# Optimization experiments

Hardware: AMD Instinct MI355X
Metric: run time of the kernel (lower is better)

Reference implementation:

```python
import jax, jax.numpy as jnp
import numpy as np

DIM = 192
HEAD_DIM = 32
HEADS = DIM // HEAD_DIM  # 6
H = W = 56
WS = 7            # window size
SS = 3            # shift size
L = WS * WS       # tokens per window = 49
NH, NW = H // WS, W // WS
NWIN = NH * NW    # windows per image = 64
SCALE = HEAD_DIM ** -0.5


def _rel_indices():
    # matches ShiftedWindowAttention.get_indices
    a = np.arange(WS)
    y1, x1, y2, x2 = np.meshgrid(a, a, a, a, indexing='ij')
    idx = (y1 - y2 + WS - 1) * (2 * WS - 1) + (x1 - x2 + WS - 1)
    return idx.reshape(-1)  # [WS^4] = [L*L]


def _shift_mask():
    # matches ShiftedWindowAttention.generate_mask -> bool [NWIN, L, L]
    region = np.zeros((H, W), dtype=np.int32)
    slices = [slice(0, -WS), slice(-WS, -SS), slice(-SS, None)]
    r = 0
    for i in slices:
        for j in slices:
            region[i, j] = r
            r += 1
    win = region.reshape(NH, WS, NW, WS).transpose(0, 2, 1, 3).reshape(NWIN, L)
    return (win[:, None, :] - win[:, :, None]) != 0


_REL_IDX = _rel_indices()
_MASK = _shift_mask()


def setup_inputs() -> dict:
    key = jax.random.key(0)
    ks = jax.random.split(key, 4)
    B = 32
    return {
        'x': jax.random.normal(ks[0], (B, H * W, DIM), jnp.float32),
        'w_qkv': jax.random.normal(ks[1], (3 * DIM, DIM), jnp.float32) * 0.02,
        'b_qkv': jnp.zeros((3 * DIM,), jnp.float32),
        'w_out': jax.random.normal(ks[2], (DIM, DIM), jnp.float32) * 0.02,
        'b_out': jnp.zeros((DIM,), jnp.float32),
        'pos_enc': jax.random.normal(ks[3], (HEADS, (2 * WS - 1) ** 2), jnp.float32) * 0.02,
    }


def reference(x, w_qkv, b_qkv, w_out, b_out, pos_enc):
    B = x.shape[0]
    # to windows (with cyclic shift)
    xg = x.reshape(B, H, W, DIM)
    xg = jnp.roll(xg, (-SS, -SS), axis=(1, 2))
    xw = xg.reshape(B, NH, WS, NW, WS, DIM).transpose(0, 1, 3, 2, 4, 5)
    xw = xw.reshape(B * NWIN, L, DIM)
    # qkv projection: torch Linear -> x @ W^T + b
    qkv = xw @ w_qkv.T + b_qkv                      # [BW, L, 3*DIM]
    qkv = qkv.reshape(B * NWIN, L, 3, HEADS, HEAD_DIM)
    qkv = qkv.transpose(2, 0, 3, 1, 4)              # [3, BW, heads, L, hd]
    q, k, v = qkv[0], qkv[1], qkv[2]
    # attention scores + gathered relative position bias
    att = jnp.einsum('whid,whjd->whij', q, k) * SCALE  # [BW, heads, L, L]
    rel = pos_enc[:, _REL_IDX].reshape(HEADS, L, L)    # gather per head
    att = att + rel
    # shift mask
    mask = jnp.asarray(_MASK)                          # [NWIN, L, L]
    att = att.reshape(B, NWIN, HEADS, L, L)
    att = jnp.where(mask[None, :, None, :, :], -jnp.inf, att)
    att = att.reshape(B * NWIN, HEADS, L, L)
    att = jax.nn.softmax(att, axis=-1)
    # weighted values, merge heads
    out = jnp.einsum('whij,whjd->whid', att, v)        # [BW, heads, L, hd]
    out = out.transpose(0, 2, 1, 3).reshape(B * NWIN, L, DIM)
    out = out @ w_out.T + b_out
    # from windows (undo shift)
    out = out.reshape(B, NH, NW, WS, WS, DIM).transpose(0, 1, 3, 2, 4, 5)
    out = out.reshape(B, H, W, DIM)
    out = jnp.roll(out, (SS, SS), axis=(1, 2))
    return out.reshape(B, H * W, DIM)
```

## Files before the change

### kernel.cpp

```cpp
#include <hip/hip_runtime.h>
#include <hip/hip_bf16.h>
#include <cstddef>
#include <cstdint>

typedef _Float16 half_t;
typedef _Float16 half8  __attribute__((ext_vector_type(8)));
typedef _Float16 half4v __attribute__((ext_vector_type(4)));
typedef float    f32x4  __attribute__((ext_vector_type(4)));

#define SCALE 0.17677669529663687f


__global__ __launch_bounds__(256) void convert_w(
    const float* __restrict__ w_qkv, const float* __restrict__ w_out,
    half_t* __restrict__ wq, half_t* __restrict__ wo)
{
    int i = blockIdx.x * 256 + threadIdx.x;
    if (i < 110592) {
        int u8 = i >> 3, e = i & 7;
        int c  = u8 & 15;
        int g  = (u8 >> 4) & 3;
        int ks = (u8 >> 6) % 6;
        int ct = u8 / 384;
        wq[i] = (half_t)w_qkv[(16 * ct + c) * 192 + ks * 32 + g * 8 + e];
    } else {
        int j = i - 110592;
        if (j < 36864) {
            int u8 = j >> 3, e = j & 7;
            int c  = u8 & 15;
            int g  = (u8 >> 4) & 3;
            int ks = (u8 >> 6) % 6;
            int q  = u8 / 384;
            wo[j] = (half_t)w_out[(16 * q + c) * 192 + ks * 32 + g * 8 + e];
        }
    }
}

__global__ __launch_bounds__(256) void build_bias(
    const float* __restrict__ pos_enc, half_t* __restrict__ mb)
{
    int idx = blockIdx.x * 256 + threadIdx.x;
    int j   = idx & 63;
    int i   = (idx >> 6) & 63;
    int hmc = idx >> 12;
    int h   = hmc % 6, mc = hmc / 6;
    float v = -60000.f;
    if (i < 49 && j < 49) {
        int yi = i / 7, xi = i - 7 * yi;
        int yj = j / 7, xj = j - 7 * yj;
        int ri = ((mc & 2) ? (yi < 4 ? 1 : 2) : 0) * 3 + ((mc & 1) ? (xi < 4 ? 1 : 2) : 0);
        int rj = ((mc & 2) ? (yj < 4 ? 1 : 2) : 0) * 3 + ((mc & 1) ? (xj < 4 ? 1 : 2) : 0);
        if (ri == rj) v = pos_enc[h * 169 + (yi - yj + 6) * 13 + (xi - xj + 6)];
    }
    mb[idx] = (half_t)v;
}

__global__ __launch_bounds__(512, 4) void swin_fused(
    const float*  __restrict__ x,
    const half_t* __restrict__ wqfrag,
    const float*  __restrict__ b_qkv,
    const half_t* __restrict__ mb16,
    const half_t* __restrict__ wofrag,
    const float*  __restrict__ b_out,
    float* __restrict__ out)
{
    __shared__ half_t sQ[2][2][64][34];
    __shared__ half_t sK[2][2][64][34];
    __shared__ half_t sV2[2][2][4][2][16][16];
    __shared__ half_t sA2[12][64][16];

    const int w    = blockIdx.x;
    const int b    = w >> 6, win = w & 63, nh = win >> 3, nw = win & 7;
    const int tid  = threadIdx.x;
    const int wave = tid >> 6, lane = tid & 63;
    const int c    = lane & 15, g = lane >> 4;
    const int cf = wave >> 1, mh = wave & 1;
    const int ti = wave & 3, hf = wave >> 2;
    const int i_tok = 16 * ti + c;
    const int mc = 2 * (nh == 7) + (nw == 7);

    half8 xf[2][6];
    #pragma unroll
    for (int t = 0; t < 2; ++t) {
        int tok = 32 * mh + 16 * t + c;
        if (tok < 49) {
            int ty = tok / 7, tx = tok - ty * 7;
            int sy = nh * 7 + ty + 3; if (sy >= 56) sy -= 56;
            int sx = nw * 7 + tx + 3; if (sx >= 56) sx -= 56;
            const float* xr = x + ((size_t)b * 3136 + sy * 56 + sx) * 192 + g * 8;
            #pragma unroll
            for (int ks = 0; ks < 6; ++ks) {
                float4 v0 = *(const float4*)(xr + ks * 32);
                float4 v1 = *(const float4*)(xr + ks * 32 + 4);
                xf[t][ks] = (half8){(half_t)v0.x, (half_t)v0.y, (half_t)v0.z, (half_t)v0.w,
                                    (half_t)v1.x, (half_t)v1.y, (half_t)v1.z, (half_t)v1.w};
            }
        } else {
            #pragma unroll
            for (int ks = 0; ks < 6; ++ks)
                xf[t][ks] = (half8){(half_t)0.f, (half_t)0.f, (half_t)0.f, (half_t)0.f,
                                    (half_t)0.f, (half_t)0.f, (half_t)0.f, (half_t)0.f};
        }
    }

    #pragma unroll
    for (int pp = 0; pp < 3; ++pp) {
        const int buf = pp & 1;

        {
            f32x4 acc[3][2];
            #pragma unroll
            for (int q = 0; q < 3; ++q) {
                acc[q][0] = (f32x4){0.f, 0.f, 0.f, 0.f};
                acc[q][1] = (f32x4){0.f, 0.f, 0.f, 0.f};
            }
            #pragma unroll
            for (int ks = 0; ks < 6; ++ks) {
                #pragma unroll
                for (int q = 0; q < 3; ++q) {
                    const int cc   = 3 * cf + q;
                    const int kind = cc >> 2, sub = cc & 3;
                    const int hh   = sub >> 1, dh = sub & 1;
                    const int ct   = kind * 12 + (2 * pp + hh) * 2 + dh;
                    half8 bF = *(const half8*)(wqfrag + (((size_t)ct * 6 + ks) * 64 + g * 16 + c) * 8);
                    acc[q][0] = __builtin_amdgcn_mfma_f32_16x16x32_f16(xf[0][ks], bF, acc[q][0], 0, 0, 0);
                    acc[q][1] = __builtin_amdgcn_mfma_f32_16x16x32_f16(xf[1][ks], bF, acc[q][1], 0, 0, 0);
                }
            }
            #pragma unroll
            for (int q = 0; q < 3; ++q) {
                const int cc   = 3 * cf + q;
                const int kind = cc >> 2, sub = cc & 3;
                const int hh   = sub >> 1, dh = sub & 1;
                const int ct   = kind * 12 + (2 * pp + hh) * 2 + dh;
                const float bias = b_qkv[16 * ct + c];
                if (kind == 2) {
                    #pragma unroll
                    for (int t = 0; t < 2; ++t) {
                        half4v pv = (half4v){(half_t)(acc[q][t][0] + bias), (half_t)(acc[q][t][1] + bias),
                                             (half_t)(acc[q][t][2] + bias), (half_t)(acc[q][t][3] + bias)};
                        *(half4v*)&sV2[buf][hh][2 * mh + t][dh][c][4 * g] = pv;
                    }
                } else {
                    #pragma unroll
                    for (int t = 0; t < 2; ++t) {
                        #pragma unroll
                        for (int r = 0; r < 4; ++r) {
                            int tok = 32 * mh + 16 * t + 4 * g + r;
                            half_t vv = (half_t)(acc[q][t][r] + bias);
                            if (kind == 0) sQ[buf][hh][tok][dh * 16 + c] = vv;
                            else           sK[buf][hh][tok][dh * 16 + c] = vv;
                        }
                    }
                }
            }
        }
        __syncthreads();

        {
            const int h = 2 * pp + hf;
            const half_t* mrow = mb16 + ((size_t)(mc * 6 + h) * 64 + i_tok) * 64;
            half4v bfr[4];
            #pragma unroll
            for (int tj = 0; tj < 4; ++tj)
                bfr[tj] = *(const half4v*)(mrow + 16 * tj + 4 * g);

            half8 qf = *(const half8*)&sQ[buf][hf][i_tok][g * 8];
            f32x4 st[4];
            #pragma unroll
            for (int tj = 0; tj < 4; ++tj) {
                half8 kf = *(const half8*)&sK[buf][hf][16 * tj + c][g * 8];
                f32x4 z = (f32x4){0.f, 0.f, 0.f, 0.f};
                st[tj] = __builtin_amdgcn_mfma_f32_16x16x32_f16(kf, qf, z, 0, 0, 0);
            }
            #pragma unroll
            for (int tj = 0; tj < 4; ++tj)
                #pragma unroll
                for (int r = 0; r < 4; ++r)
                    st[tj][r] = st[tj][r] * SCALE + (float)bfr[tj][r];

            float m = st[0][0];
            #pragma unroll
            for (int tj = 0; tj < 4; ++tj)
                #pragma unroll
                for (int r = 0; r < 4; ++r) m = fmaxf(m, st[tj][r]);
            m = fmaxf(m, __shfl_xor(m, 16));
            m = fmaxf(m, __shfl_xor(m, 32));
            float sum = 0.f;
            #pragma unroll
            for (int tj = 0; tj < 4; ++tj)
                #pragma unroll
                for (int r = 0; r < 4; ++r) {
                    float e = __expf(st[tj][r] - m);
                    st[tj][r] = e;
                    sum += e;
                }
            sum += __shfl_xor(sum, 16);
            sum += __shfl_xor(sum, 32);
            float inv = 1.0f / sum;
            half4v pa[4];
            #pragma unroll
            for (int tj = 0; tj < 4; ++tj)
                pa[tj] = (half4v){(half_t)(st[tj][0] * inv), (half_t)(st[tj][1] * inv),
                                  (half_t)(st[tj][2] * inv), (half_t)(st[tj][3] * inv)};

            f32x4 o0 = (f32x4){0.f, 0.f, 0.f, 0.f};
            f32x4 o1 = (f32x4){0.f, 0.f, 0.f, 0.f};
            #pragma unroll
            for (int tj = 0; tj < 4; ++tj) {
                half4v v0 = *(const half4v*)&sV2[buf][hf][tj][0][c][4 * g];
                half4v v1 = *(const half4v*)&sV2[buf][hf][tj][1][c][4 * g];
                o0 = __builtin_amdgcn_mfma_f32_16x16x16f16(v0, pa[tj], o0, 0, 0, 0);
                o1 = __builtin_amdgcn_mfma_f32_16x16x16f16(v1, pa[tj], o1, 0, 0, 0);
            }
            *(half4v*)&sA2[2 * h][i_tok][4 * g] =
                (half4v){(half_t)o0[0], (half_t)o0[1], (half_t)o0[2], (half_t)o0[3]};
            *(half4v*)&sA2[2 * h + 1][i_tok][4 * g] =
                (half4v){(half_t)o1[0], (half_t)o1[1], (half_t)o1[2], (half_t)o1[3]};
        }
    }
    __syncthreads();

    {
        f32x4 pacc[6];
        float bo[6];
        #pragma unroll
        for (int q = 0; q < 6; ++q) {
            pacc[q] = (f32x4){0.f, 0.f, 0.f, 0.f};
            bo[q] = b_out[16 * (6 * hf + q) + c];
        }
        #pragma unroll
        for (int ks = 0; ks < 6; ++ks) {
            half8 aF = *(const half8*)&sA2[2 * ks + (g >> 1)][i_tok][(g & 1) * 8];
            #pragma unroll
            for (int q = 0; q < 6; ++q) {
                int ct = 6 * hf + q;
                half8 bF = *(const half8*)(wofrag + ((size_t)(ct * 6 + ks) * 64 + lane) * 8);
                pacc[q] = __builtin_amdgcn_mfma_f32_16x16x32_f16(aF, bF, pacc[q], 0, 0, 0);
            }
        }
        #pragma unroll
        for (int r = 0; r < 4; ++r) {
            int tok = 16 * ti + g * 4 + r;
            if (tok < 49) {
                int ty = tok / 7, tx = tok - ty * 7;
                int dy = nh * 7 + ty + 3; if (dy >= 56) dy -= 56;
                int dx = nw * 7 + tx + 3; if (dx >= 56) dx -= 56;
                float* op = out + ((size_t)b * 3136 + dy * 56 + dx) * 192;
                #pragma unroll
                for (int q = 0; q < 6; ++q)
                    op[16 * (6 * hf + q) + c] = pacc[q][r] + bo[q];
            }
        }
    }
}

extern "C" void kernel_launch(void* const* d_in, const int* in_sizes, int n_in,
                              void* d_out, int out_size, void* d_ws, size_t ws_size,
                              hipStream_t stream) {
    const float* x       = (const float*)d_in[0];
    const float* w_qkv   = (const float*)d_in[1];
    const float* b_qkv   = (const float*)d_in[2];
    const float* w_out   = (const float*)d_in[3];
    const float* b_out   = (const float*)d_in[4];
    const float* pos_enc = (const float*)d_in[5];
    float* out = (float*)d_out;

    half_t* wqf  = (half_t*)d_ws;
    half_t* wof  = (half_t*)((char*)d_ws + 221184);
    half_t* mb16 = (half_t*)((char*)d_ws + 294912);

    convert_w<<<dim3(576), dim3(256), 0, stream>>>(w_qkv, w_out, wqf, wof);
    build_bias<<<dim3(384), dim3(256), 0, stream>>>(pos_enc, mb16);
    swin_fused<<<dim3(2048), dim3(512), 0, stream>>>(
        x, wqf, b_qkv, mb16, wof, b_out, out);
}
```

Before: 148.6 us.

## Keep Q in registers, store K/V in MFMA fragment layout, one barrier

Each wave now projects Q, K and V for its own 16-token tile and three heads at once, keeping Q fragments in registers and writing K/V into shared memory already in MFMA operand order. The padded last tile (tokens 48..63) is stored as a single broadcast row. This replaces the three per-head-pair phases, each ending in a __syncthreads, with a single barrier. It also prefetches the mask/bias rows one head ahead and writes the attention output directly in the fragment layout the output projection reads. The cost is more register pressure from 6 Q fragments, and redundant weight loads since each wave reads its own heads' weights.

```diff
diff --git a/kernel.cpp b/kernel.cpp
--- a/kernel.cpp
+++ b/kernel.cpp
@@ -64,158 +64,212 @@
     const float*  __restrict__ b_out,
     float* __restrict__ out)
 {
-    __shared__ half_t sQ[2][2][64][34];
-    __shared__ half_t sK[2][2][64][34];
-    __shared__ half_t sV2[2][2][4][2][16][16];
-    __shared__ half_t sA2[12][64][16];
+    __shared__ __align__(16) half_t sKf[6 * 2 * 3 * 256];
+    __shared__ __align__(16) half_t sVf[6 * 2 * 3 * 256];
+    __shared__ __align__(16) half_t sKt[6 * 2 * 16];
+    __shared__ __align__(16) half_t sVt[6 * 2 * 16];
+    __shared__ __align__(16) half_t sAf[6 * 4 * 64 * 8];
 
     const int w    = blockIdx.x;
     const int b    = w >> 6, win = w & 63, nh = win >> 3, nw = win & 7;
     const int tid  = threadIdx.x;
     const int wave = tid >> 6, lane = tid & 63;
     const int c    = lane & 15, g = lane >> 4;
-    const int cf = wave >> 1, mh = wave & 1;
-    const int ti = wave & 3, hf = wave >> 2;
+    const int ti   = wave & 3, hf = wave >> 2;
     const int i_tok = 16 * ti + c;
-    const int mc = 2 * (nh == 7) + (nw == 7);
-
-    half8 xf[2][6];
+    const int mc   = 2 * (nh == 7) + (nw == 7);
+
+    half8 xf[6];
+    if (i_tok < 49) {
+        int ty = i_tok / 7, tx = i_tok - ty * 7;
+        int sy = nh * 7 + ty + 3; if (sy >= 56) sy -= 56;
+        int sx = nw * 7 + tx + 3; if (sx >= 56) sx -= 56;
+        const float* xr = x + ((size_t)b * 3136 + sy * 56 + sx) * 192 + g * 8;
+        #pragma unroll
+        for (int ks = 0; ks < 6; ++ks) {
+            float4 v0 = *(const float4*)(xr + ks * 32);
+            float4 v1 = *(const float4*)(xr + ks * 32 + 4);
+            xf[ks] = (half8){(half_t)v0.x, (half_t)v0.y, (half_t)v0.z, (half_t)v0.w,
+                             (half_t)v1.x, (half_t)v1.y, (half_t)v1.z, (half_t)v1.w};
+        }
+    } else {
+        #pragma unroll
+        for (int ks = 0; ks < 6; ++ks)
+            xf[ks] = (half8){(half_t)0.f, (half_t)0.f, (half_t)0.f, (half_t)0.f,
+                             (half_t)0.f, (half_t)0.f, (half_t)0.f, (half_t)0.f};
+    }
+
+    half4v qf[3][2];
     #pragma unroll
-    for (int t = 0; t < 2; ++t) {
-        int tok = 32 * mh + 16 * t + c;
-        if (tok < 49) {
-            int ty = tok / 7, tx = tok - ty * 7;
-            int sy = nh * 7 + ty + 3; if (sy >= 56) sy -= 56;
-            int sx = nw * 7 + tx + 3; if (sx >= 56) sx -= 56;
-            const float* xr = x + ((size_t)b * 3136 + sy * 56 + sx) * 192 + g * 8;
-            #pragma unroll
-            for (int ks = 0; ks < 6; ++ks) {
-                float4 v0 = *(const float4*)(xr + ks * 32);
-                float4 v1 = *(const float4*)(xr + ks * 32 + 4);
-                xf[t][ks] = (half8){(half_t)v0.x, (half_t)v0.y, (half_t)v0.z, (half_t)v0.w,
-                                    (half_t)v1.x, (half_t)v1.y, (half_t)v1.z, (half_t)v1.w};
-            }
-        } else {
+    for (int p = 0; p < 3; ++p) {
+        #pragma unroll
+        for (int dh = 0; dh < 2; ++dh) {
+            const int h  = 3 * hf + p;
+            const int ct = h * 2 + dh;
+            const half_t* wp = wqfrag + ((size_t)ct * 384 + lane) * 8;
+            half8 bfm[6];
+            #pragma unroll
+            for (int ks = 0; ks < 6; ++ks) bfm[ks] = *(const half8*)(wp + ks * 512);
+            f32x4 a0 = (f32x4){0.f, 0.f, 0.f, 0.f};
             #pragma unroll
             for (int ks = 0; ks < 6; ++ks)
-                xf[t][ks] = (half8){(half_t)0.f, (half_t)0.f, (half_t)0.f, (half_t)0.f,
-                                    (half_t)0.f, (half_t)0.f, (half_t)0.f, (half_t)0.f};
+                a0 = __builtin_amdgcn_mfma_f32_16x16x32_f16(bfm[ks], xf[ks], a0, 0, 0, 0);
+            float4 bq = *(const float4*)(b_qkv + 16 * ct + 4 * g);
+            half4v pv = (half4v){(half_t)(a0[0] + bq.x), (half_t)(a0[1] + bq.y),
+                                 (half_t)(a0[2] + bq.z), (half_t)(a0[3] + bq.w)};
+            if (ti < 3) {
+                qf[p][dh] = pv;
+            } else {
+                union { half4v h; int i2[2]; } u; u.h = pv;
+                u.i2[0] = __shfl(u.i2[0], lane & 48);
+                u.i2[1] = __shfl(u.i2[1], lane & 48);
+                qf[p][dh] = u.h;
+            }
         }
     }
 
     #pragma unroll
-    for (int pp = 0; pp < 3; ++pp) {
-        const int buf = pp & 1;
-
+    for (int p = 0; p < 3; ++p) {
+        #pragma unroll
+        for (int dh = 0; dh < 2; ++dh) {
+            const int h  = 3 * hf + p;
+            const int ct = 12 + h * 2 + dh;
+            const half_t* wp = wqfrag + ((size_t)ct * 384 + lane) * 8;
+            half8 bfm[6];
+            #pragma unroll
+            for (int ks = 0; ks < 6; ++ks) bfm[ks] = *(const half8*)(wp + ks * 512);
+            f32x4 a0 = (f32x4){0.f, 0.f, 0.f, 0.f};
+            #pragma unroll
+            for (int ks = 0; ks < 6; ++ks)
+                a0 = __builtin_amdgcn_mfma_f32_16x16x32_f16(bfm[ks], xf[ks], a0, 0, 0, 0);
+            float4 bq = *(const float4*)(b_qkv + 16 * ct + 4 * g);
+            half4v pv = (half4v){(half_t)(a0[0] + bq.x), (half_t)(a0[1] + bq.y),
+                                 (half_t)(a0[2] + bq.z), (half_t)(a0[3] + bq.w)};
+            if (ti < 3) {
+                *(half4v*)&sKf[h * 1536 + dh * 768 + ti * 256 + lane * 4] = pv;
+            } else if (c == 0) {
+                *(half4v*)&sKt[(h * 2 + dh) * 16 + 4 * g] = pv;
+            }
+        }
+    }
+
+    #pragma unroll
+    for (int p = 0; p < 3; ++p) {
+        #pragma unroll
+        for (int dh = 0; dh < 2; ++dh) {
+            const int h  = 3 * hf + p;
+            const int ct = 24 + h * 2 + dh;
+            const half_t* wp = wqfrag + ((size_t)ct * 384 + lane) * 8;
+            half8 bfm[6];
+            #pragma unroll
+            for (int ks = 0; ks < 6; ++ks) bfm[ks] = *(const half8*)(wp + ks * 512);
+            f32x4 a0 = (f32x4){0.f, 0.f, 0.f, 0.f};
+            #pragma unroll
+            for (int ks = 0; ks < 6; ++ks)
+                a0 = __builtin_amdgcn_mfma_f32_16x16x32_f16(xf[ks], bfm[ks], a0, 0, 0, 0);
+            const float bv = b_qkv[16 * ct + c];
+            if (ti < 3) {
+                half4v pv = (half4v){(half_t)(a0[0] + bv), (half_t)(a0[1] + bv),
+                                     (half_t)(a0[2] + bv), (half_t)(a0[3] + bv)};
+                *(half4v*)&sVf[h * 1536 + dh * 768 + ti * 256 + lane * 4] = pv;
+            } else if (g == 0) {
+                sVt[(h * 2 + dh) * 16 + c] = (half_t)(a0[0] + bv);
+            }
+        }
+    }
+    __syncthreads();
+
+    half4v bA[4], bB[4];
+    {
+        const half_t* mrow = mb16 + ((size_t)(mc * 6 + 3 * hf) * 64 + i_tok) * 64;
+        #pragma unroll
+        for (int tj = 0; tj < 4; ++tj)
+            bA[tj] = *(const half4v*)(mrow + 16 * tj + 4 * g);
+    }
+
+    #pragma unroll
+    for (int p = 0; p < 3; ++p) {
+        const int h = 3 * hf + p;
+        if (p == 0) {
+            const half_t* mrow = mb16 + ((size_t)(mc * 6 + h + 1) * 64 + i_tok) * 64;
+            #pragma unroll
+            for (int tj = 0; tj < 4; ++tj) bB[tj] = *(const half4v*)(mrow + 16 * tj + 4 * g);
+        }
+        if (p == 1) {
+            const half_t* mrow = mb16 + ((size_t)(mc * 6 + h + 1) * 64 + i_tok) * 64;
+            #pragma unroll
+            for (int tj = 0; tj < 4; ++tj) bA[tj] = *(const half4v*)(mrow + 16 * tj + 4 * g);
+        }
+        const half4v* bf = (p == 1) ? bB : bA;
+
+        f32x4 st[4];
+        #pragma unroll
+        for (int tj = 0; tj < 4; ++tj) {
+            half4v ka0, ka1;
+            if (tj < 3) {
+                ka0 = *(const half4v*)&sKf[h * 1536 + 0 * 768 + tj * 256 + lane * 4];
+                ka1 = *(const half4v*)&sKf[h * 1536 + 1 * 768 + tj * 256 + lane * 4];
+            } else {
+                ka0 = *(const half4v*)&sKt[(h * 2 + 0) * 16 + 4 * g];
+                ka1 = *(const half4v*)&sKt[(h * 2 + 1) * 16 + 4 * g];
+            }
+            f32x4 z = (f32x4){0.f, 0.f, 0.f, 0.f};
+            z = __builtin_amdgcn_mfma_f32_16x16x16f16(ka0, qf[p][0], z, 0, 0, 0);
+            st[tj] = __builtin_amdgcn_mfma_f32_16x16x16f16(ka1, qf[p][1], z, 0, 0, 0);
+        }
+        #pragma unroll
+        for (int tj = 0; tj < 4; ++tj)
+            #pragma unroll
+            for (int r = 0; r < 4; ++r)
+                st[tj][r] = st[tj][r] * SCALE + (float)bf[tj][r];
+
+        float m = st[0][0];
+        #pragma unroll
+        for (int tj = 0; tj < 4; ++tj)
+            #pragma unroll
+            for (int r = 0; r < 4; ++r) m = fmaxf(m, st[tj][r]);
+        m = fmaxf(m, __shfl_xor(m, 16));
+        m = fmaxf(m, __shfl_xor(m, 32));
+        float sum = 0.f;
+        #pragma unroll
+        for (int tj = 0; tj < 4; ++tj)
+            #pragma unroll
+            for (int r = 0; r < 4; ++r) {
+                float e = __expf(st[tj][r] - m);
+                st[tj][r] = e;
+                sum += e;
+            }
+        sum += __shfl_xor(sum, 16);
+        sum += __shfl_xor(sum, 32);
+        float inv = 1.0f / sum;
+        half4v pa[4];
+        #pragma unroll
+        for (int tj = 0; tj < 4; ++tj)
+            pa[tj] = (half4v){(half_t)(st[tj][0] * inv), (half_t)(st[tj][1] * inv),
+                              (half_t)(st[tj][2] * inv), (half_t)(st[tj][3] * inv)};
+
+        f32x4 o0 = (f32x4){0.f, 0.f, 0.f, 0.f};
+        f32x4 o1 = (f32x4){0.f, 0.f, 0.f, 0.f};
+        #pragma unroll
+        for (int tj = 0; tj < 3; ++tj) {
+            half4v v0 = *(const half4v*)&sVf[h * 1536 + 0 * 768 + tj * 256 + lane * 4];
+            half4v v1 = *(const half4v*)&sVf[h * 1536 + 1 * 768 + tj * 256 + lane * 4];
+            o0 = __builtin_amdgcn_mfma_f32_16x16x16f16(v0, pa[tj], o0, 0, 0, 0);
+            o1 = __builtin_amdgcn_mfma_f32_16x16x16f16(v1, pa[tj], o1, 0, 0, 0);
+        }
         {
-            f32x4 acc[3][2];
-            #pragma unroll
-            for (int q = 0; q < 3; ++q) {
-                acc[q][0] = (f32x4){0.f, 0.f, 0.f, 0.f};
-                acc[q][1] = (f32x4){0.f, 0.f, 0.f, 0.f};
-            }
-            #pragma unroll
-            for (int ks = 0; ks < 6; ++ks) {
-                #pragma unroll
-                for (int q = 0; q < 3; ++q) {
-                    const int cc   = 3 * cf + q;
-                    const int kind = cc >> 2, sub = cc & 3;
-                    const int hh   = sub >> 1, dh = sub & 1;
-                    const int ct   = kind * 12 + (2 * pp + hh) * 2 + dh;
-                    half8 bF = *(const half8*)(wqfrag + (((size_t)ct * 6 + ks) * 64 + g * 16 + c) * 8);
-                    acc[q][0] = __builtin_amdgcn_mfma_f32_16x16x32_f16(xf[0][ks], bF, acc[q][0], 0, 0, 0);
-                    acc[q][1] = __builtin_amdgcn_mfma_f32_16x16x32_f16(xf[1][ks], bF, acc[q][1], 0, 0, 0);
-                }
-            }
-            #pragma unroll
-            for (int q = 0; q < 3; ++q) {
-                const int cc   = 3 * cf + q;
-                const int kind = cc >> 2, sub = cc & 3;
-                const int hh   = sub >> 1, dh = sub & 1;
-                const int ct   = kind * 12 + (2 * pp + hh) * 2 + dh;
-                const float bias = b_qkv[16 * ct + c];
-                if (kind == 2) {
-                    #pragma unroll
-                    for (int t = 0; t < 2; ++t) {
-                        half4v pv = (half4v){(half_t)(acc[q][t][0] + bias), (half_t)(acc[q][t][1] + bias),
-                                             (half_t)(acc[q][t][2] + bias), (half_t)(acc[q][t][3] + bias)};
-                        *(half4v*)&sV2[buf][hh][2 * mh + t][dh][c][4 * g] = pv;
-                    }
-                } else {
-                    #pragma unroll
-                    for (int t = 0; t < 2; ++t) {
-                        #pragma unroll
-                        for (int r = 0; r < 4; ++r) {
-                            int tok = 32 * mh + 16 * t + 4 * g + r;
-                            half_t vv = (half_t)(acc[q][t][r] + bias);
-                            if (kind == 0) sQ[buf][hh][tok][dh * 16 + c] = vv;
-                            else           sK[buf][hh][tok][dh * 16 + c] = vv;
-                        }
-                    }
-                }
-            }
-        }
-        __syncthreads();
-
+            half_t tv0 = sVt[(h * 2 + 0) * 16 + c];
+            half_t tv1 = sVt[(h * 2 + 1) * 16 + c];
+            half4v v30 = (half4v){tv0, tv0, tv0, tv0};
+            half4v v31 = (half4v){tv1, tv1, tv1, tv1};
+            o0 = __builtin_amdgcn_mfma_f32_16x16x16f16(v30, pa[3], o0, 0, 0, 0);
+            o1 = __builtin_amdgcn_mfma_f32_16x16x16f16(v31, pa[3], o1, 0, 0, 0);
+        }
         {
-            const int h = 2 * pp + hf;
-            const half_t* mrow = mb16 + ((size_t)(mc * 6 + h) * 64 + i_tok) * 64;
-            half4v bfr[4];
-            #pragma unroll
-            for (int tj = 0; tj < 4; ++tj)
-                bfr[tj] = *(const half4v*)(mrow + 16 * tj + 4 * g);
-
-            half8 qf = *(const half8*)&sQ[buf][hf][i_tok][g * 8];
-            f32x4 st[4];
-            #pragma unroll
-            for (int tj = 0; tj < 4; ++tj) {
-                half8 kf = *(const half8*)&sK[buf][hf][16 * tj + c][g * 8];
-                f32x4 z = (f32x4){0.f, 0.f, 0.f, 0.f};
-                st[tj] = __builtin_amdgcn_mfma_f32_16x16x32_f16(kf, qf, z, 0, 0, 0);
-            }
-            #pragma unroll
-            for (int tj = 0; tj < 4; ++tj)
-                #pragma unroll
-                for (int r = 0; r < 4; ++r)
-                    st[tj][r] = st[tj][r] * SCALE + (float)bfr[tj][r];
-
-            float m = st[0][0];
-            #pragma unroll
-            for (int tj = 0; tj < 4; ++tj)
-                #pragma unroll
-                for (int r = 0; r < 4; ++r) m = fmaxf(m, st[tj][r]);
-            m = fmaxf(m, __shfl_xor(m, 16));
-            m = fmaxf(m, __shfl_xor(m, 32));
-            float sum = 0.f;
-            #pragma unroll
-            for (int tj = 0; tj < 4; ++tj)
-                #pragma unroll
-                for (int r = 0; r < 4; ++r) {
-                    float e = __expf(st[tj][r] - m);
-                    st[tj][r] = e;
-                    sum += e;
-                }
-            sum += __shfl_xor(sum, 16);
-            sum += __shfl_xor(sum, 32);
-            float inv = 1.0f / sum;
-            half4v pa[4];
-            #pragma unroll
-            for (int tj = 0; tj < 4; ++tj)
-                pa[tj] = (half4v){(half_t)(st[tj][0] * inv), (half_t)(st[tj][1] * inv),
-                                  (half_t)(st[tj][2] * inv), (half_t)(st[tj][3] * inv)};
-
-            f32x4 o0 = (f32x4){0.f, 0.f, 0.f, 0.f};
-            f32x4 o1 = (f32x4){0.f, 0.f, 0.f, 0.f};
-            #pragma unroll
-            for (int tj = 0; tj < 4; ++tj) {
-                half4v v0 = *(const half4v*)&sV2[buf][hf][tj][0][c][4 * g];
-                half4v v1 = *(const half4v*)&sV2[buf][hf][tj][1][c][4 * g];
-                o0 = __builtin_amdgcn_mfma_f32_16x16x16f16(v0, pa[tj], o0, 0, 0, 0);
-                o1 = __builtin_amdgcn_mfma_f32_16x16x16f16(v1, pa[tj], o1, 0, 0, 0);
-            }
-            *(half4v*)&sA2[2 * h][i_tok][4 * g] =
+            int base = (((h * 4 + ti) * 64 + (g >> 1) * 16 + c) << 3) + (g & 1) * 4;
+            *(half4v*)&sAf[base] =
                 (half4v){(half_t)o0[0], (half_t)o0[1], (half_t)o0[2], (half_t)o0[3]};
-            *(half4v*)&sA2[2 * h + 1][i_tok][4 * g] =
+            *(half4v*)&sAf[base + 256] =
                 (half4v){(half_t)o1[0], (half_t)o1[1], (half_t)o1[2], (half_t)o1[3]};
         }
     }
@@ -231,7 +285,7 @@
         }
         #pragma unroll
         for (int ks = 0; ks < 6; ++ks) {
-            half8 aF = *(const half8*)&sA2[2 * ks + (g >> 1)][i_tok][(g & 1) * 8];
+            half8 aF = *(const half8*)&sAf[((ks * 4 + ti) * 64 + lane) * 8];
             #pragma unroll
             for (int q = 0; q < 6; ++q) {
                 int ct = 6 * hf + q;
```

After: 135.2 us. 9.0% less time.
